# Kernel tuning notes

Measured on AMD Instinct MI355X. Metric: run time of the kernel, lower is better.

Reference implementation:

```python
import jax, jax.numpy as jnp
import numpy as np
from jax import lax

BASE = 10000.0

def _rope(x):
    # x: (b, h, w, c). Faithful to torch RoPE: angles depend only on one spatial
    # axis (h,k_max) and broadcast against the *w* axis of x (valid since h==w).
    b, h, w, c = x.shape
    k_max = c // 2
    theta = 1.0 / (BASE ** (jnp.arange(k_max, dtype=x.dtype) / k_max))  # (k_max,)
    angles = jnp.arange(h, dtype=x.dtype)[:, None] * theta              # (h, k_max)
    cos = jnp.cos(angles)[None, None]  # (1,1,h,k_max) -> broadcasts over w axis
    sin = jnp.sin(angles)[None, None]
    xr = x.reshape(b, h, w, k_max, 2)
    re, im = xr[..., 0], xr[..., 1]
    out = jnp.stack([re * cos - im * sin, re * sin + im * cos], axis=-1)
    return out.reshape(b, h, w, c)


def setup_inputs() -> dict:
    key = jax.random.key(0)
    k1, k2, k3 = jax.random.split(key, 3)
    B, C, H, W = 8, 128, 160, 160
    x = jax.random.normal(k1, (B, C, H, W), dtype=jnp.float32)
    qk_w = jax.random.normal(k2, (2 * C, C), dtype=jnp.float32) * 0.02
    qk_b = jnp.zeros((2 * C,), dtype=jnp.float32)
    lepe_w = jax.random.normal(k3, (C, 1, 3, 3), dtype=jnp.float32) * 0.1
    lepe_b = jnp.zeros((C,), dtype=jnp.float32)
    return {"x": x, "qk_w": qk_w, "qk_b": qk_b,
            "lepe_w": lepe_w, "lepe_b": lepe_b, "num_heads": 8}


def reference(x, qk_w, qk_b, lepe_w, lepe_b, num_heads):
    b, c, H, W = x.shape
    n = H * W
    hd = c // num_heads
    # raw row-major reshape (B,C,H,W) -> (B,N,C), matching torch .reshape
    xf = x.reshape(b, n, c)
    qk = (xf @ qk_w.T + qk_b).reshape(b, n, 2, c)
    q = jax.nn.elu(qk[:, :, 0]) + 1.0
    k = jax.nn.elu(qk[:, :, 1]) + 1.0
    v = xf
    q_rope = _rope(q.reshape(b, H, W, c)).reshape(b, n, num_heads, hd).transpose(0, 2, 1, 3)
    k_rope = _rope(k.reshape(b, H, W, c)).reshape(b, n, num_heads, hd).transpose(0, 2, 1, 3)
    qh = q.reshape(b, n, num_heads, hd).transpose(0, 2, 1, 3)  # (b,h,n,d)
    kh = k.reshape(b, n, num_heads, hd).transpose(0, 2, 1, 3)
    vh = v.reshape(b, n, num_heads, hd).transpose(0, 2, 1, 3)
    z = 1.0 / (jnp.einsum('bhnd,bhd->bhn', qh, kh.mean(axis=2)) + 1e-6)  # (b,h,n)
    scale = float(n) ** -0.5
    kv = jnp.einsum('bhnd,bhne->bhde', k_rope * scale, vh * scale)  # (b,h,d,d)
    out = jnp.einsum('bhnd,bhde->bhne', q_rope, kv) * z[..., None]  # (b,h,n,d)
    out = out.transpose(0, 2, 1, 3).reshape(b, n, c)
    # LePE: depthwise 3x3 conv on v laid out as image
    vimg = vh.transpose(0, 2, 1, 3).reshape(b, H, W, c).transpose(0, 3, 1, 2)  # (b,c,H,W)
    lepe = lax.conv_general_dilated(vimg, lepe_w, (1, 1), 'SAME',
                                    feature_group_count=c)
    lepe = lepe + lepe_b[None, :, None, None]
    out = out + lepe.transpose(0, 2, 3, 1).reshape(b, n, c)
    return out.transpose(0, 2, 1).reshape(b, c, H, W)
```

## Files before the change

### kernel.cpp

```cpp
#include <hip/hip_runtime.h>
#include <cstdint>
#include <cstddef>

#define NB 8
#define NC 128
#define NHH 160
#define NWW 160
#define NNN (NHH*NWW)
#define TILE_R 64
#define TPB (NNN/TILE_R)
#define NSLOTS 32
#define LN_B 0.14391156511f

typedef __attribute__((ext_vector_type(8))) short short8v;
typedef __attribute__((ext_vector_type(4))) short short4v;
typedef __attribute__((ext_vector_type(4))) float f32x4;
union B64x2 { short8v v8; short4v v4[2]; ushort u[8]; uint w[4]; };

__device__ __forceinline__ float elup1(float y){ return y>0.f? y+1.f : __expf(y); }
__device__ __forceinline__ ushort f2bf(float f){ uint x=__float_as_uint(f); x+=0x7fffu+((x>>16)&1u); return (ushort)(x>>16); }
__device__ __forceinline__ uint cvtpk(float lo, float hi){
  uint r;
  asm("v_cvt_pk_bf16_f32 %0, %1, %2" : "=v"(r) : "v"(lo), "v"(hi));
  return r;
}
__device__ __forceinline__ float frcp(float x){
  float r;
  asm("v_rcp_f32 %0, %1" : "=v"(r) : "v"(x));
  return r;
}
__device__ __forceinline__ float bfhi(uint u){ return __uint_as_float(u & 0xffff0000u); }
__device__ __forceinline__ float bflo(uint u){ return __uint_as_float(u << 16); }
__device__ __forceinline__ int divH(int i){ return ((i >> 5) * 6554) >> 15; }
__device__ __forceinline__ int iclamp(int v, int lo, int hi){ return v<lo?lo:(v>hi?hi:v); }

__global__ __launch_bounds__(256) void kprep(
    const float* __restrict__ qk_w, ushort* __restrict__ wbf,
    float2* __restrict__ rtab, float* __restrict__ zreg)
{
  const int id = blockIdx.x*256 + threadIdx.x;
  if (id < 2*NC*NC) wbf[id] = f2bf(qk_w[id]);
  if (id < NWW*64) {
    const int ww = id >> 6, f = id & 63;
    const float th = __expf(-LN_B * (float)f);
    float s, c; __sincosf((float)ww * th, &s, &c);
    rtab[id] = make_float2(c, s);
  }
  #pragma unroll
  for (int j = 0; j < 17; ++j)
    zreg[id + j*32768] = 0.f;
}

__global__ __launch_bounds__(256, 3) void k1_proj(
    const float* __restrict__ x, const ushort* __restrict__ wbf,
    const float* __restrict__ qk_b, const float2* __restrict__ rtab,
    ushort* __restrict__ qu, float* __restrict__ kv_part,
    float* __restrict__ ksum_part)
{
  __shared__ __align__(16) ushort xbf[64][136];
  __shared__ __align__(16) ushort wch[64][136];
  __shared__ __align__(16) ushort xtp[64][68];
  __shared__ __align__(16) ushort krt[64][68];
  __shared__ float ksum_lds[NC];

  const int blk  = ((blockIdx.x & 7) * (NB*TPB/8)) + (blockIdx.x >> 3);
  const int b    = blk / TPB;
  const int tile = blk - b * TPB;
  const int i0   = tile * TILE_R;
  const int tid  = threadIdx.x;
  const int lane = tid & 63;
  const int wv   = tid >> 6;
  const int lg   = lane >> 4;
  const int ll   = lane & 15;
  const float* xb = x + (size_t)b*NNN*NC + (size_t)i0*NC;

  {
    const float4* src = (const float4*)xb;
    for (int f = tid; f < TILE_R*NC/4; f += 256) {
      float4 v = src[f];
      uint w0 = cvtpk(v.x, v.y), w1 = cvtpk(v.z, v.w);
      *(uint2*)&xbf[f >> 5][(f & 31) << 2] = make_uint2(w0, w1);
    }
  }
  if (tid < NC) ksum_lds[tid] = 0.f;
  __syncthreads();

  f32x4 kvacc[2];
  kvacc[0] = (f32x4){0.f,0.f,0.f,0.f};
  kvacc[1] = (f32x4){0.f,0.f,0.f,0.f};
  const int row0 = (wv<<4) + (lg<<2);

  int wfr4[4];
  #pragma unroll
  for (int r = 0; r < 4; ++r) {
    const int i = i0 + row0 + r;
    wfr4[r] = i - divH(i)*NWW;
  }

  for (int chunk = 0; chunk < 4; ++chunk) {
    if (chunk) __syncthreads();
    {
      const uint4* wsrc = (const uint4*)(wbf + (size_t)(chunk*64)*NC);
      for (int f = tid; f < 1024; f += 256)
        *(uint4*)&wch[f >> 4][(f & 15) << 3] = wsrc[f];
    }
    if (chunk >= 2) {
      #pragma unroll
      for (int t = 0; t < 2; ++t) {
        const int task = tid + (t << 8);
        const int c = task & 63, rg = task >> 6;
        ushort tmp[8];
        #pragma unroll
        for (int k2 = 0; k2 < 8; ++k2) tmp[k2] = xbf[(rg<<3)+k2][((chunk-2)<<6)+c];
        *(ushort4*)&xtp[c][(rg<<3)]   = make_ushort4(tmp[0],tmp[1],tmp[2],tmp[3]);
        *(ushort4*)&xtp[c][(rg<<3)+4] = make_ushort4(tmp[4],tmp[5],tmp[6],tmp[7]);
      }
    }
    __syncthreads();

    f32x4 acc[4];
    acc[0]=acc[1]=acc[2]=acc[3]=(f32x4){0.f,0.f,0.f,0.f};
    #pragma unroll
    for (int ks = 0; ks < 4; ++ks) {
      short8v a = *(const short8v*)&xbf[(wv<<4) + ll][(ks<<5) + (lg<<3)];
      #pragma unroll
      for (int nt = 0; nt < 4; ++nt) {
        short8v bb = *(const short8v*)&wch[(nt<<4) + ll][(ks<<5) + (lg<<3)];
        acc[nt] = __builtin_amdgcn_mfma_f32_16x16x32_bf16(a, bb, acc[nt], 0, 0, 0);
      }
    }

    if (chunk < 2) {
      ushort* qb = qu + ((size_t)b*NNN + (size_t)i0)*NC;
      #pragma unroll
      for (int nt = 0; nt < 4; ++nt) {
        const int cg = (chunk<<6) + (nt<<4) + ll;
        const float bias = qk_b[cg];
        #pragma unroll
        for (int r = 0; r < 4; ++r)
          qb[(size_t)(row0 + r)*NC + cg] = f2bf(elup1(acc[nt][r] + bias));
      }
    } else {
      #pragma unroll
      for (int nt = 0; nt < 4; ++nt) {
        const int kcl = (nt<<4) + ll;
        const int kc  = ((chunk-2)<<6) + kcl;
        const float bias = qk_b[NC + kc];
        float kk[4]; float ss = 0.f;
        #pragma unroll
        for (int r = 0; r < 4; ++r) { kk[r] = elup1(acc[nt][r] + bias); ss += kk[r]; }
        atomicAdd(&ksum_lds[kc], ss);
        ushort rb[4];
        #pragma unroll
        for (int r = 0; r < 4; ++r) {
          float p = __shfl_xor(kk[r], 1);
          float2 cs = rtab[wfr4[r]*64 + (kc >> 1)];
          float kr = (kc & 1) ? (p*cs.y + kk[r]*cs.x) : (kk[r]*cs.x - p*cs.y);
          rb[r] = f2bf(kr);
        }
        *(uint*)&krt[kcl][row0]   = (uint)rb[0] | ((uint)rb[1] << 16);
        *(uint*)&krt[kcl][row0+2] = (uint)rb[2] | ((uint)rb[3] << 16);
      }
      __syncthreads();

      const int e2 = chunk - 2;
      #pragma unroll
      for (int ks = 0; ks < 2; ++ks) {
        const int rb2 = (ks<<5) + (lg<<3);
        B64x2 ua, ub;
        ua.v4[0] = *(const short4v*)&krt[(wv<<4) + ll][rb2];
        ua.v4[1] = *(const short4v*)&krt[(wv<<4) + ll][rb2+4];
        ub.v4[0] = *(const short4v*)&xtp[(wv<<4) + ll][rb2];
        ub.v4[1] = *(const short4v*)&xtp[(wv<<4) + ll][rb2+4];
        kvacc[e2] = __builtin_amdgcn_mfma_f32_16x16x32_bf16(ua.v8, ub.v8, kvacc[e2], 0, 0, 0);
      }
    }
  }

  const int slot = blk & (NSLOTS-1);
  {
    float* kvp = kv_part + ((size_t)b*NSLOTS + slot) * 2048;
    #pragma unroll
    for (int e2 = 0; e2 < 2; ++e2) {
      const int h = (e2<<2) + wv;
      #pragma unroll
      for (int r = 0; r < 4; ++r) {
        const int d = (lg<<2) + r;
        atomicAdd(&kvp[(h<<8) + (d<<4) + ll], kvacc[e2][r]);
      }
    }
  }
  if (tid < NC) atomicAdd(&ksum_part[((size_t)b*NSLOTS + slot)*NC + tid], ksum_lds[tid]);
}

__global__ __launch_bounds__(256) void k_reduce(
    const float* __restrict__ kv_part, const float* __restrict__ ksum_part,
    float* __restrict__ kvf, float* __restrict__ kmean)
{
  const int gtid = blockIdx.x * 256 + threadIdx.x;
  const int b = gtid >> 11;
  const int cidx = gtid & 2047;
  float s = 0.f;
  for (int sl = 0; sl < NSLOTS; ++sl)
    s += kv_part[((size_t)b*NSLOTS + sl)*2048 + cidx];
  kvf[(size_t)b*2048 + cidx] = s * (1.f/25600.f);
  if (cidx < NC) {
    float t = 0.f;
    for (int sl = 0; sl < NSLOTS; ++sl)
      t += ksum_part[((size_t)b*NSLOTS + sl)*NC + cidx];
    kmean[(size_t)b*NC + cidx] = t * (1.f/25600.f);
  }
}

__global__ __launch_bounds__(256, 2) void k2_out(
    const float* __restrict__ x, const ushort* __restrict__ qu,
    const float* __restrict__ kvf, const float* __restrict__ kmean,
    const float* __restrict__ lepe_w, const float* __restrict__ lepe_b,
    const float2* __restrict__ rtab, float* __restrict__ outp)
{
  __shared__ __align__(16) ushort qu_s[64*136];

  const int blk  = ((blockIdx.x & 7) * (NB*TPB/8)) + (blockIdx.x >> 3);
  const int b    = blk / TPB;
  const int tile = blk - b * TPB;
  const int i0   = tile * TILE_R;
  const int tid  = threadIdx.x;
  const int lane = tid & 63;
  const int wv   = tid >> 6;
  const int lg   = lane >> 4;
  const int ll   = lane & 15;
  const float* xb = x + (size_t)b*NNN*NC;

  {
    const uint4* qsrc = (const uint4*)(qu + ((size_t)b*NNN + (size_t)i0)*NC);
    #pragma unroll
    for (int t = 0; t < 4; ++t) {
      const int f = tid + (t << 8);
      uint4 v = qsrc[f];
      const int row = f >> 4, c8 = f & 15;
      *(uint4*)&qu_s[row*136 + ((c8 ^ (row & 7)) << 3)] = v;
    }
  }
  __syncthreads();

  const bool interior = (i0 >= 192) && (i0 <= NNN - 225);

  int wfa[4];
  #pragma unroll
  for (int mt = 0; mt < 4; ++mt) {
    const int i = i0 + (mt<<4) + ll;
    wfa[mt] = i - divH(i)*NWW;
  }

  #pragma unroll
  for (int hs = 0; hs < 2; ++hs) {
    const int h  = wv + (hs<<2);
    const int ch = (h<<4) + ll;
    B64x2 kb, kz;
    kb.v8 = (short8v){0,0,0,0,0,0,0,0};
    kz.v8 = (short8v){0,0,0,0,0,0,0,0};
    if (lg < 2) {
      const float* kvp = kvf + (size_t)b*2048 + (h<<8) + ll;
      #pragma unroll
      for (int j2 = 0; j2 < 4; ++j2) {
        float f0 = kvp[(((lg<<3) + 2*j2    ) << 4)];
        float f1 = kvp[(((lg<<3) + 2*j2 + 1) << 4)];
        kb.w[j2] = cvtpk(f0, f1);
      }
      const float* kmp = kmean + (size_t)b*NC + (h<<4) + (lg<<3);
      #pragma unroll
      for (int j2 = 0; j2 < 4; ++j2)
        kz.w[j2] = cvtpk(kmp[2*j2], kmp[2*j2+1]);
    }
    f32x4 pacc[4], zacc[4];
    #pragma unroll
    for (int mt = 0; mt < 4; ++mt) {
      short8v a  = (short8v){0,0,0,0,0,0,0,0};
      short8v au = (short8v){0,0,0,0,0,0,0,0};
      if (lg < 2) {
        const int row = (mt<<4) + ll;
        const int off = row*136 + ((((h<<1) + lg) ^ (row & 7)) << 3);
        B64x2 uq;
        uq.v8 = *(const short8v*)&qu_s[off];
        au = uq.v8;
        const float2* tp = rtab + wfa[mt]*64 + (h<<3) + (lg<<2);
        B64x2 ra;
        #pragma unroll
        for (int j = 0; j < 4; ++j) {
          float2 cs = tp[j];
          float e = bflo(uq.w[j]), o = bfhi(uq.w[j]);
          ra.w[j] = cvtpk(e*cs.x - o*cs.y, e*cs.y + o*cs.x);
        }
        a = ra.v8;
      }
      pacc[mt] = __builtin_amdgcn_mfma_f32_16x16x32_bf16(
          a,  kb.v8, (f32x4){0.f,0.f,0.f,0.f}, 0, 0, 0);
      zacc[mt] = __builtin_amdgcn_mfma_f32_16x16x32_bf16(
          au, kz.v8, (f32x4){0.f,0.f,0.f,0.f}, 0, 0, 0);
    }
    float wl[9];
    #pragma unroll
    for (int t = 0; t < 9; ++t) wl[t] = lepe_w[ch*9 + t];
    const float lb = lepe_b[ch];
    const float* xc = xb + ch;

    if (interior) {
      #pragma unroll
      for (int mt = 0; mt < 4; ++mt) {
        const int lrow = (mt<<4) + (lg<<2);
        const int ib   = i0 + lrow;
        const float* pu = xc + (size_t)(ib-161)*NC;
        const float* pm = xc + (size_t)(ib-1  )*NC;
        const float* pd = xc + (size_t)(ib+159)*NC;
        float mu[6], mm[6], md[6];
        #pragma unroll
        for (int j = 0; j < 6; ++j) {
          mu[j] = pu[j*NC]; mm[j] = pm[j*NC]; md[j] = pd[j*NC];
        }
        int ww = ib - divH(ib)*NWW;
        float4 ov;
        #pragma unroll
        for (int r = 0; r < 4; ++r) {
          const float zz = frcp(zacc[mt][r] + 1e-6f);
          const float fx0 = ww > 0   ? 1.f : 0.f;
          const float fx2 = ww < 159 ? 1.f : 0.f;
          float lp = lb;
          lp += fx0*(wl[0]*mu[r] + wl[3]*mm[r] + wl[6]*md[r]);
          lp +=     (wl[1]*mu[r+1] + wl[4]*mm[r+1] + wl[7]*md[r+1]);
          lp += fx2*(wl[2]*mu[r+2] + wl[5]*mm[r+2] + wl[8]*md[r+2]);
          (&ov.x)[r] = pacc[mt][r]*zz + lp;
          ww = (ww == NWW-1) ? 0 : ww + 1;
        }
        *(float4*)(outp + ((size_t)b*NC + ch)*NNN + ib) = ov;
      }
    } else {
      #pragma unroll
      for (int mt = 0; mt < 4; ++mt) {
        const int lrow = (mt<<4) + (lg<<2);
        const int ib   = i0 + lrow;
        float mu[6], mm[6], md[6];
        #pragma unroll
        for (int j = 0; j < 6; ++j) {
          const int im = ib - 1 + j;
          mu[j] = xc[(size_t)(iclamp(im-160, 0, NNN-1)) * NC];
          mm[j] = xc[(size_t)(iclamp(im,     0, NNN-1)) * NC];
          md[j] = xc[(size_t)(iclamp(im+160, 0, NNN-1)) * NC];
        }
        int hh = divH(ib);
        int ww = ib - hh*NWW;
        float4 ov;
        #pragma unroll
        for (int r = 0; r < 4; ++r) {
          const float zz = frcp(zacc[mt][r] + 1e-6f);
          const float fy0 = hh > 0   ? 1.f : 0.f;
          const float fy2 = hh < 159 ? 1.f : 0.f;
          const float fx0 = ww > 0   ? 1.f : 0.f;
          const float fx2 = ww < 159 ? 1.f : 0.f;
          float lp = lb;
          lp += fy0*(fx0*wl[0]*mu[r] + wl[1]*mu[r+1] + fx2*wl[2]*mu[r+2]);
          lp +=     (fx0*wl[3]*mm[r] + wl[4]*mm[r+1] + fx2*wl[5]*mm[r+2]);
          lp += fy2*(fx0*wl[6]*md[r] + wl[7]*md[r+1] + fx2*wl[8]*md[r+2]);
          (&ov.x)[r] = pacc[mt][r]*zz + lp;
          const int cy = (ww == NWW-1) ? 1 : 0;
          hh += cy;
          ww = cy ? 0 : ww + 1;
        }
        *(float4*)(outp + ((size_t)b*NC + ch)*NNN + ib) = ov;
      }
    }
  }
}

extern "C" void kernel_launch(void* const* d_in, const int* in_sizes, int n_in,
                              void* d_out, int out_size, void* d_ws, size_t ws_size,
                              hipStream_t stream) {
  const float* x      = (const float*)d_in[0];
  const float* qk_w   = (const float*)d_in[1];
  const float* qk_b   = (const float*)d_in[2];
  const float* lepe_w = (const float*)d_in[3];
  const float* lepe_b = (const float*)d_in[4];
  float* outp = (float*)d_out;

  float* kv_part   = (float*)d_ws;
  float* ksum_part = kv_part + (size_t)NB*NSLOTS*2048;
  float* kvf       = ksum_part + (size_t)NB*NSLOTS*NC;
  float* kmean     = kvf + (size_t)NB*2048;
  float2* rtab     = (float2*)(kmean + (size_t)NB*NC);
  ushort* wbf      = (ushort*)(rtab + (size_t)NWW*64);
  ushort* qubuf    = wbf + (size_t)2*NC*NC;

  hipLaunchKernelGGL(kprep, dim3(128), dim3(256), 0, stream,
                     qk_w, wbf, rtab, kv_part);
  hipLaunchKernelGGL(k1_proj, dim3(NB*TPB), dim3(256), 0, stream,
                     x, wbf, qk_b, rtab, qubuf, kv_part, ksum_part);
  hipLaunchKernelGGL(k_reduce, dim3(64), dim3(256), 0, stream,
                     kv_part, ksum_part, kvf, kmean);
  hipLaunchKernelGGL(k2_out, dim3(NB*TPB), dim3(256), 0, stream,
                     x, qubuf, kvf, kmean, lepe_w, lepe_b, rtab, outp);
}
```

Before: 164.5 us.

## Drop weight LDS staging, stage Q tile in LDS for coalesced stores, raise occupancy

The projection kernel no longer copies weight chunks into shared memory. MFMA B-fragments are now read directly from global bf16 weights, which should hit in cache. Q outputs are first written into a swizzled shared buffer, then stored to global as coalesced uint4 rows instead of scattered 2-byte stores. The buffer is pre-swizzled so the consumer kernel no longer needs to XOR-swizzle its Q load. Freeing the weight buffer shrinks LDS use, and launch bounds go from 3 to 4 blocks per CU, at the cost of more global/L2 traffic for weight fragments.

```diff
diff --git a/kernel.cpp b/kernel.cpp
--- a/kernel.cpp
+++ b/kernel.cpp
@@ -51,17 +51,17 @@
     zreg[id + j*32768] = 0.f;
 }
 
-__global__ __launch_bounds__(256, 3) void k1_proj(
+__global__ __launch_bounds__(256, 4) void k1_proj(
     const float* __restrict__ x, const ushort* __restrict__ wbf,
     const float* __restrict__ qk_b, const float2* __restrict__ rtab,
     ushort* __restrict__ qu, float* __restrict__ kv_part,
     float* __restrict__ ksum_part)
 {
   __shared__ __align__(16) ushort xbf[64][136];
-  __shared__ __align__(16) ushort wch[64][136];
-  __shared__ __align__(16) ushort xtp[64][68];
-  __shared__ __align__(16) ushort krt[64][68];
+  __shared__ __align__(16) ushort aux[8704];
   __shared__ float ksum_lds[NC];
+  ushort* xtp = aux;
+  ushort* krt = aux + 4352;
 
   const int blk  = ((blockIdx.x & 7) * (NB*TPB/8)) + (blockIdx.x >> 3);
   const int b    = blk / TPB;
@@ -85,9 +85,6 @@
   if (tid < NC) ksum_lds[tid] = 0.f;
   __syncthreads();
 
-  f32x4 kvacc[2];
-  kvacc[0] = (f32x4){0.f,0.f,0.f,0.f};
-  kvacc[1] = (f32x4){0.f,0.f,0.f,0.f};
   const int row0 = (wv<<4) + (lg<<2);
 
   int wfr4[4];
@@ -97,26 +94,63 @@
     wfr4[r] = i - divH(i)*NWW;
   }
 
-  for (int chunk = 0; chunk < 4; ++chunk) {
+  #pragma unroll
+  for (int chunk = 0; chunk < 2; ++chunk) {
+    f32x4 acc[4];
+    acc[0]=acc[1]=acc[2]=acc[3]=(f32x4){0.f,0.f,0.f,0.f};
+    #pragma unroll
+    for (int ks = 0; ks < 4; ++ks) {
+      short8v a = *(const short8v*)&xbf[(wv<<4) + ll][(ks<<5) + (lg<<3)];
+      #pragma unroll
+      for (int nt = 0; nt < 4; ++nt) {
+        short8v bb = *(const short8v*)(wbf +
+            (size_t)((chunk<<6) + (nt<<4) + ll)*NC + (ks<<5) + (lg<<3));
+        acc[nt] = __builtin_amdgcn_mfma_f32_16x16x32_bf16(a, bb, acc[nt], 0, 0, 0);
+      }
+    }
+    #pragma unroll
+    for (int nt = 0; nt < 4; ++nt) {
+      const int cg = (chunk<<6) + (nt<<4) + ll;
+      const float bias = qk_b[cg];
+      #pragma unroll
+      for (int r = 0; r < 4; ++r) {
+        const int row = row0 + r;
+        aux[row*136 + (((cg>>3) ^ (row & 7))<<3) + (cg&7)] =
+            f2bf(elup1(acc[nt][r] + bias));
+      }
+    }
+  }
+  __syncthreads();
+
+  {
+    uint4* qdst = (uint4*)(qu + ((size_t)b*NNN + (size_t)i0)*NC);
+    #pragma unroll
+    for (int t = 0; t < 4; ++t) {
+      const int f = tid + (t << 8);
+      const int row = f >> 4, c8 = f & 15;
+      qdst[f] = *(const uint4*)&aux[row*136 + (c8<<3)];
+    }
+  }
+  __syncthreads();
+
+  f32x4 kvacc[2];
+  kvacc[0] = (f32x4){0.f,0.f,0.f,0.f};
+  kvacc[1] = (f32x4){0.f,0.f,0.f,0.f};
+
+  for (int chunk = 0; chunk < 2; ++chunk) {
     if (chunk) __syncthreads();
     {
-      const uint4* wsrc = (const uint4*)(wbf + (size_t)(chunk*64)*NC);
-      for (int f = tid; f < 1024; f += 256)
-        *(uint4*)&wch[f >> 4][(f & 15) << 3] = wsrc[f];
-    }
-    if (chunk >= 2) {
       #pragma unroll
       for (int t = 0; t < 2; ++t) {
         const int task = tid + (t << 8);
         const int c = task & 63, rg = task >> 6;
         ushort tmp[8];
         #pragma unroll
-        for (int k2 = 0; k2 < 8; ++k2) tmp[k2] = xbf[(rg<<3)+k2][((chunk-2)<<6)+c];
-        *(ushort4*)&xtp[c][(rg<<3)]   = make_ushort4(tmp[0],tmp[1],tmp[2],tmp[3]);
-        *(ushort4*)&xtp[c][(rg<<3)+4] = make_ushort4(tmp[4],tmp[5],tmp[6],tmp[7]);
-      }
-    }
-    __syncthreads();
+        for (int k2 = 0; k2 < 8; ++k2) tmp[k2] = xbf[(rg<<3)+k2][(chunk<<6)+c];
+        *(ushort4*)&xtp[c*68 + (rg<<3)]     = make_ushort4(tmp[0],tmp[1],tmp[2],tmp[3]);
+        *(ushort4*)&xtp[c*68 + (rg<<3) + 4] = make_ushort4(tmp[4],tmp[5],tmp[6],tmp[7]);
+      }
+    }
 
     f32x4 acc[4];
     acc[0]=acc[1]=acc[2]=acc[3]=(f32x4){0.f,0.f,0.f,0.f};
@@ -125,55 +159,43 @@
       short8v a = *(const short8v*)&xbf[(wv<<4) + ll][(ks<<5) + (lg<<3)];
       #pragma unroll
       for (int nt = 0; nt < 4; ++nt) {
-        short8v bb = *(const short8v*)&wch[(nt<<4) + ll][(ks<<5) + (lg<<3)];
+        short8v bb = *(const short8v*)(wbf +
+            (size_t)(NC + (chunk<<6) + (nt<<4) + ll)*NC + (ks<<5) + (lg<<3));
         acc[nt] = __builtin_amdgcn_mfma_f32_16x16x32_bf16(a, bb, acc[nt], 0, 0, 0);
       }
     }
 
-    if (chunk < 2) {
-      ushort* qb = qu + ((size_t)b*NNN + (size_t)i0)*NC;
-      #pragma unroll
-      for (int nt = 0; nt < 4; ++nt) {
-        const int cg = (chunk<<6) + (nt<<4) + ll;
-        const float bias = qk_b[cg];
-        #pragma unroll
-        for (int r = 0; r < 4; ++r)
-          qb[(size_t)(row0 + r)*NC + cg] = f2bf(elup1(acc[nt][r] + bias));
-      }
-    } else {
-      #pragma unroll
-      for (int nt = 0; nt < 4; ++nt) {
-        const int kcl = (nt<<4) + ll;
-        const int kc  = ((chunk-2)<<6) + kcl;
-        const float bias = qk_b[NC + kc];
-        float kk[4]; float ss = 0.f;
-        #pragma unroll
-        for (int r = 0; r < 4; ++r) { kk[r] = elup1(acc[nt][r] + bias); ss += kk[r]; }
-        atomicAdd(&ksum_lds[kc], ss);
-        ushort rb[4];
-        #pragma unroll
-        for (int r = 0; r < 4; ++r) {
-          float p = __shfl_xor(kk[r], 1);
-          float2 cs = rtab[wfr4[r]*64 + (kc >> 1)];
-          float kr = (kc & 1) ? (p*cs.y + kk[r]*cs.x) : (kk[r]*cs.x - p*cs.y);
-          rb[r] = f2bf(kr);
-        }
-        *(uint*)&krt[kcl][row0]   = (uint)rb[0] | ((uint)rb[1] << 16);
-        *(uint*)&krt[kcl][row0+2] = (uint)rb[2] | ((uint)rb[3] << 16);
-      }
-      __syncthreads();
-
-      const int e2 = chunk - 2;
-      #pragma unroll
-      for (int ks = 0; ks < 2; ++ks) {
-        const int rb2 = (ks<<5) + (lg<<3);
-        B64x2 ua, ub;
-        ua.v4[0] = *(const short4v*)&krt[(wv<<4) + ll][rb2];
-        ua.v4[1] = *(const short4v*)&krt[(wv<<4) + ll][rb2+4];
-        ub.v4[0] = *(const short4v*)&xtp[(wv<<4) + ll][rb2];
-        ub.v4[1] = *(const short4v*)&xtp[(wv<<4) + ll][rb2+4];
-        kvacc[e2] = __builtin_amdgcn_mfma_f32_16x16x32_bf16(ua.v8, ub.v8, kvacc[e2], 0, 0, 0);
-      }
+    #pragma unroll
+    for (int nt = 0; nt < 4; ++nt) {
+      const int kcl = (nt<<4) + ll;
+      const int kc  = (chunk<<6) + kcl;
+      const float bias = qk_b[NC + kc];
+      float kk[4]; float ss = 0.f;
+      #pragma unroll
+      for (int r = 0; r < 4; ++r) { kk[r] = elup1(acc[nt][r] + bias); ss += kk[r]; }
+      atomicAdd(&ksum_lds[kc], ss);
+      ushort rb[4];
+      #pragma unroll
+      for (int r = 0; r < 4; ++r) {
+        float p = __shfl_xor(kk[r], 1);
+        float2 cs = rtab[wfr4[r]*64 + (kc >> 1)];
+        float kr = (kc & 1) ? (p*cs.y + kk[r]*cs.x) : (kk[r]*cs.x - p*cs.y);
+        rb[r] = f2bf(kr);
+      }
+      *(uint*)&krt[kcl*68 + row0]     = (uint)rb[0] | ((uint)rb[1] << 16);
+      *(uint*)&krt[kcl*68 + row0 + 2] = (uint)rb[2] | ((uint)rb[3] << 16);
+    }
+    __syncthreads();
+
+    #pragma unroll
+    for (int ks = 0; ks < 2; ++ks) {
+      const int rb2 = (ks<<5) + (lg<<3);
+      B64x2 ua, ub;
+      ua.v4[0] = *(const short4v*)&krt[((wv<<4) + ll)*68 + rb2];
+      ua.v4[1] = *(const short4v*)&krt[((wv<<4) + ll)*68 + rb2 + 4];
+      ub.v4[0] = *(const short4v*)&xtp[((wv<<4) + ll)*68 + rb2];
+      ub.v4[1] = *(const short4v*)&xtp[((wv<<4) + ll)*68 + rb2 + 4];
+      kvacc[chunk] = __builtin_amdgcn_mfma_f32_16x16x32_bf16(ua.v8, ub.v8, kvacc[chunk], 0, 0, 0);
     }
   }
 
@@ -238,7 +260,7 @@
       const int f = tid + (t << 8);
       uint4 v = qsrc[f];
       const int row = f >> 4, c8 = f & 15;
-      *(uint4*)&qu_s[row*136 + ((c8 ^ (row & 7)) << 3)] = v;
+      *(uint4*)&qu_s[row*136 + (c8 << 3)] = v;
     }
   }
   __syncthreads();
```

Result: slower. 197.4 us (+20.0%).
